# Kernel tuning notes

Measured on AMD Instinct MI355X. Metric: run time of the kernel, lower is better.

The kernel has to match this reference:

```python
import jax, jax.numpy as jnp
import numpy as np

TEMPERATURE = 8.0  # sqrt(d_k) with d_k=64

def setup_inputs() -> dict:
    key = jax.random.key(0)
    k1, k2, k3, k4 = jax.random.split(key, 4)
    B, L, D = 64, 1024, 64  # B = batch*n_heads
    q = jax.random.normal(k1, (B, L, D), dtype=jnp.float32)
    k = jax.random.normal(k2, (B, L, D), dtype=jnp.float32)
    v = jax.random.normal(k3, (B, L, D), dtype=jnp.float32)
    mask = jax.random.randint(k4, (B, L, L), 0, 2).astype(jnp.bool_)
    return {"q": q, "k": k, "v": v, "mask": mask}

def reference(q, k, v, mask):
    # scores: [B, Lq, Lk]
    attn = jnp.einsum('bqd,bkd->bqk', q, k) / TEMPERATURE
    attn = jnp.where(mask, -jnp.inf, attn)
    attn = jax.nn.softmax(attn, axis=2)
    output = jnp.einsum('bqk,bkd->bqd', attn, v)
    return (output, attn)
```

## Files before the change

kernel.cpp:

```cpp
#include <hip/hip_runtime.h>

#define B_ 64
#define L_ 1024
#define D_ 64
#define QT 16

typedef _Float16 f16;
typedef __attribute__((ext_vector_type(8))) _Float16 f16x8;
typedef __attribute__((ext_vector_type(4))) _Float16 f16x4;
typedef __attribute__((ext_vector_type(4))) float f32x4;

#define WS_KH 0u
#define WS_KL 8388608u
#define WS_VT 16777216u
#define WS_NEED 25165824u

#define MFMA16(A, B, C) __builtin_amdgcn_mfma_f32_16x16x32_f16((A), (B), (C), 0, 0, 0)

__global__ __launch_bounds__(256)
void prep_kv(const float* __restrict__ kk, const float* __restrict__ v,
             f16* __restrict__ kh, f16* __restrict__ kl, f16* __restrict__ vt) {
    __shared__ f16 tile[64][72];
    if (blockIdx.x < 2048) {
        const int i = (blockIdx.x * 256 + threadIdx.x) * 8;
        float4 f0 = *(const float4*)(kk + i);
        float4 f1 = *(const float4*)(kk + i + 4);
        float fv[8] = {f0.x, f0.y, f0.z, f0.w, f1.x, f1.y, f1.z, f1.w};
        f16x8 h, lo;
        #pragma unroll
        for (int j = 0; j < 8; ++j) {
            float x = fv[j] * 0.125f;
            f16 hh = (f16)x;
            h[j] = hh;
            lo[j] = (f16)(x - (float)hh);
        }
        *(f16x8*)(kh + i) = h;
        *(f16x8*)(kl + i) = lo;
    } else {
        const int bb = blockIdx.x - 2048;
        const int b = bb >> 4, kt = bb & 15;
        const int r = threadIdx.x >> 2, c0 = (threadIdx.x & 3) * 16;
        const float* vp = v + (size_t)(b * L_ + kt * 64 + r) * D_ + c0;
        float4 g0 = *(const float4*)vp;
        float4 g1 = *(const float4*)(vp + 4);
        float4 g2 = *(const float4*)(vp + 8);
        float4 g3 = *(const float4*)(vp + 12);
        float fv[16] = {g0.x, g0.y, g0.z, g0.w, g1.x, g1.y, g1.z, g1.w,
                        g2.x, g2.y, g2.z, g2.w, g3.x, g3.y, g3.z, g3.w};
        #pragma unroll
        for (int j = 0; j < 16; ++j) tile[r][c0 + j] = (f16)fv[j];
        __syncthreads();
        f16x8 o0, o1;
        #pragma unroll
        for (int j = 0; j < 8; ++j) { o0[j] = tile[c0 + j][r]; o1[j] = tile[c0 + 8 + j][r]; }
        f16* op = vt + (size_t)(b * 64 + r) * 1024 + kt * 64 + c0;
        *(f16x8*)op = o0;
        *(f16x8*)(op + 8) = o1;
    }
}


template<bool E4>
__device__ __forceinline__ void sdpa_body(
    const float* __restrict__ q, const f16* __restrict__ kh,
    const f16* __restrict__ kl, const f16* __restrict__ vt,
    const unsigned char* __restrict__ mask,
    float* __restrict__ out, float* __restrict__ attn,
    f16* __restrict__ ST, float (*wsumP)[QT], float* __restrict__ OL)
{
    const int tid = threadIdx.x;
    const int l = tid & 63, w = tid >> 6;
    const int lr = l & 15, lg = l >> 4;
    const int bid = blockIdx.x;
    const int b = bid >> 6, qt = bid & 63;
    const int qbase = b * L_ + qt * QT;
    const int kq = w * 256;
    const int wbase = w * 4096;
    const int swx = (lr & 7) << 3;

    f16x8 aqh0, aqh1, aql0, aql1;
    {
        const float* qp = q + (size_t)(qbase + lr) * D_;
        float4 f0 = *(const float4*)(qp + lg * 8);
        float4 f1 = *(const float4*)(qp + lg * 8 + 4);
        float4 f2 = *(const float4*)(qp + 32 + lg * 8);
        float4 f3 = *(const float4*)(qp + 32 + lg * 8 + 4);
        float fa[8] = {f0.x, f0.y, f0.z, f0.w, f1.x, f1.y, f1.z, f1.w};
        float fb[8] = {f2.x, f2.y, f2.z, f2.w, f3.x, f3.y, f3.z, f3.w};
        #pragma unroll
        for (int j = 0; j < 8; ++j) {
            f16 h = (f16)fa[j]; aqh0[j] = h; aql0[j] = (f16)(fa[j] - (float)h);
            h = (f16)fb[j];     aqh1[j] = h; aql1[j] = (f16)(fb[j] - (float)h);
        }
    }

    const size_t mrow = (size_t)(qbase + lr) * L_ + kq + lg * 4;
    int4 mq[4]; uchar4 mu[4];
    #pragma unroll
    for (int t = 0; t < 4; ++t) {
        if (E4) mq[t] = *(const int4*)((const int*)mask + mrow + t * 16);
        else    mu[t] = *(const uchar4*)(mask + mrow + t * 16);
    }

    const f16* khp = kh + (size_t)(b * L_ + kq + lr) * D_ + lg * 8;
    const f16* klp = kl + (size_t)(b * L_ + kq + lr) * D_ + lg * 8;
    f16x8 kc0 = *(const f16x8*)khp, kc1 = *(const f16x8*)(khp + 32);
    f16x8 lc0 = *(const f16x8*)klp, lc1 = *(const f16x8*)(klp + 32);

    float rsum = 0.f;

    #pragma unroll
    for (int c = 0; c < 16; ++c) {
        f16x8 kn0, kn1, ln0, ln1;
        if (c < 15) {
            const f16* p1 = khp + (c + 1) * 1024;
            const f16* p2 = klp + (c + 1) * 1024;
            kn0 = *(const f16x8*)p1; kn1 = *(const f16x8*)(p1 + 32);
            ln0 = *(const f16x8*)p2; ln1 = *(const f16x8*)(p2 + 32);
        }
        f32x4 acc = {0.f, 0.f, 0.f, 0.f};
        acc = MFMA16(kc0, aqh0, acc);
        acc = MFMA16(kc1, aqh1, acc);
        acc = MFMA16(kc0, aql0, acc);
        acc = MFMA16(kc1, aql1, acc);
        acc = MFMA16(lc0, aqh0, acc);
        acc = MFMA16(lc1, aqh1, acc);
        int mm[4];
        if (E4) { mm[0] = mq[c & 3].x; mm[1] = mq[c & 3].y;
                  mm[2] = mq[c & 3].z; mm[3] = mq[c & 3].w; }
        else    { mm[0] = mu[c & 3].x; mm[1] = mu[c & 3].y;
                  mm[2] = mu[c & 3].z; mm[3] = mu[c & 3].w; }
        f16x4 qd;
        #pragma unroll
        for (int r = 0; r < 4; ++r) {
            float e = mm[r] ? 0.f : __expf(acc[r]);
            rsum += e;
            qd[r] = (f16)e;
        }
        *(f16x4*)&ST[(wbase + lr * 256 + c * 16 + lg * 4) ^ swx] = qd;
        if (c + 4 < 16) {
            if (E4) mq[c & 3] = *(const int4*)((const int*)mask + mrow + (c + 4) * 16);
            else    mu[c & 3] = *(const uchar4*)(mask + mrow + (c + 4) * 16);
        }
        if (c < 15) { kc0 = kn0; kc1 = kn1; lc0 = ln0; lc1 = ln1; }
    }

    asm volatile("s_waitcnt lgkmcnt(0)" ::: "memory");
    __builtin_amdgcn_sched_barrier(0);
    f16x8 pa[8];
    #pragma unroll
    for (int t = 0; t < 8; ++t)
        pa[t] = *(const f16x8*)&ST[(wbase + lr * 256 + t * 32 + lg * 8) ^ swx];

    rsum += __shfl_xor(rsum, 16);
    rsum += __shfl_xor(rsum, 32);
    if (l < 16) wsumP[w][lr] = rsum;
    __syncthreads();

    const float inv = 1.0f / (wsumP[0][lr] + wsumP[1][lr] + wsumP[2][lr] + wsumP[3][lr]);

    const f16* vtb = vt + (size_t)b * 64 * 1024 + kq + lg * 8;
    float* ap = attn + (size_t)(qbase + lr) * L_ + kq + lg * 8;
    f32x4 acc4[4] = {{0,0,0,0},{0,0,0,0},{0,0,0,0},{0,0,0,0}};
    f16x8 bc[4];
    #pragma unroll
    for (int nt = 0; nt < 4; ++nt)
        bc[nt] = *(const f16x8*)(vtb + (size_t)(nt * 16 + lr) * 1024);

    #pragma unroll
    for (int t = 0; t < 8; ++t) {
        f16x8 bn[4];
        if (t < 7) {
            #pragma unroll
            for (int nt = 0; nt < 4; ++nt)
                bn[nt] = *(const f16x8*)(vtb + (size_t)(nt * 16 + lr) * 1024 + (t + 1) * 32);
        }
        f32x4 p0, p1;
        p0[0] = (float)pa[t][0] * inv; p0[1] = (float)pa[t][1] * inv;
        p0[2] = (float)pa[t][2] * inv; p0[3] = (float)pa[t][3] * inv;
        p1[0] = (float)pa[t][4] * inv; p1[1] = (float)pa[t][5] * inv;
        p1[2] = (float)pa[t][6] * inv; p1[3] = (float)pa[t][7] * inv;
        *(f32x4*)(ap + t * 32)     = p0;
        *(f32x4*)(ap + t * 32 + 4) = p1;
        #pragma unroll
        for (int nt = 0; nt < 4; ++nt)
            acc4[nt] = MFMA16(pa[t], bc[nt], acc4[nt]);
        if (t < 7) {
            #pragma unroll
            for (int nt = 0; nt < 4; ++nt) bc[nt] = bn[nt];
        }
    }

    #pragma unroll
    for (int nt = 0; nt < 4; ++nt) {
        #pragma unroll
        for (int r = 0; r < 4; ++r)
            OL[w * (16 * 68) + (lg * 4 + r) * 68 + nt * 16 + lr] = acc4[nt][r];
    }
    __syncthreads();
    {
        const int row = tid >> 4, c4 = (tid & 15) * 4;
        f32x4 o = {0.f, 0.f, 0.f, 0.f};
        #pragma unroll
        for (int ww = 0; ww < 4; ++ww) {
            const float* p = &OL[ww * (16 * 68) + row * 68 + c4];
            o[0] += p[0]; o[1] += p[1]; o[2] += p[2]; o[3] += p[3];
        }
        const float invr = 1.0f / (wsumP[0][row] + wsumP[1][row] + wsumP[2][row] + wsumP[3][row]);
        f32x4 r = {o[0] * invr, o[1] * invr, o[2] * invr, o[3] * invr};
        *(f32x4*)(out + (size_t)(qbase + row) * D_ + c4) = r;
    }
}

__global__ __launch_bounds__(256, 4)
void sdpa_main(const float* __restrict__ q, const f16* __restrict__ kh,
               const f16* __restrict__ kl, const f16* __restrict__ vt,
               const unsigned char* __restrict__ mask,
               float* __restrict__ out, float* __restrict__ attn)
{
    __shared__ __align__(16) char smem[32768];
    __shared__ float wsumP[4][QT];

    unsigned det = 0;
    {
        const unsigned* mw = (const unsigned*)mask;
        #pragma unroll
        for (int i = 0; i < 32; ++i) det |= mw[i];
    }
    const bool elem4 = (det <= 1u) || (det == 0x3F800000u);

    if (elem4)
        sdpa_body<true>(q, kh, kl, vt, mask, out, attn, (f16*)smem, wsumP, (float*)smem);
    else
        sdpa_body<false>(q, kh, kl, vt, mask, out, attn, (f16*)smem, wsumP, (float*)smem);
}


__device__ __forceinline__ int sidx(int row, int col) {
    return row * 1024 + ((((col >> 3) ^ (row & 7)) << 3) | (col & 7));
}

__global__ __launch_bounds__(256, 4)
void sdpa_fallback(const float* __restrict__ q, const float* __restrict__ kk,
                   const float* __restrict__ v, const unsigned char* __restrict__ mask,
                   float* __restrict__ out, float* __restrict__ attn)
{
    __shared__ f16 S[QT * 1024];
    __shared__ float wmax[4][QT];
    __shared__ float wsum[QT];

    const int tid = threadIdx.x;
    const int l = tid & 63, w = tid >> 6;
    const int lr = l & 15, lg = l >> 4;
    const int bid = blockIdx.x;
    const int b = bid >> 6, qt = bid & 63;
    const int qbase = b * L_ + qt * QT;

    unsigned det = 0;
    {
        const unsigned* mw = (const unsigned*)mask;
        #pragma unroll
        for (int i = 0; i < 32; ++i) det |= mw[i];
    }
    const bool elem4 = (det <= 1u) || (det == 0x3F800000u);

    f16x8 aqh[2], aql[2];
    {
        const float* qp = q + (size_t)(qbase + lr) * D_;
        #pragma unroll
        for (int s = 0; s < 2; ++s) {
            float4 f0 = *(const float4*)(qp + s * 32 + lg * 8);
            float4 f1 = *(const float4*)(qp + s * 32 + lg * 8 + 4);
            float fv[8] = {f0.x, f0.y, f0.z, f0.w, f1.x, f1.y, f1.z, f1.w};
            #pragma unroll
            for (int j = 0; j < 8; ++j) {
                f16 h = (f16)fv[j];
                aqh[s][j] = h;
                aql[s][j] = (f16)(fv[j] - (float)h);
            }
        }
    }

    float vmax[4] = {-INFINITY, -INFINITY, -INFINITY, -INFINITY};
    const float* kb = kk + (size_t)(b * L_ + w * 16 + lr) * D_ + lg * 8;
    const size_t mrowbase = (size_t)(qbase + lg * 4) * L_ + w * 16 + lr;

    float4 kc[4];
    kc[0] = *(const float4*)kb;
    kc[1] = *(const float4*)(kb + 4);
    kc[2] = *(const float4*)(kb + 32);
    kc[3] = *(const float4*)(kb + 36);
    int mcur[4], mnxt[4];
    #pragma unroll
    for (int r2 = 0; r2 < 4; ++r2) {
        if (elem4) {
            mcur[r2] = ((const int*)mask)[mrowbase + (size_t)r2 * L_];
            mnxt[r2] = ((const int*)mask)[mrowbase + (size_t)r2 * L_ + 64];
        } else {
            mcur[r2] = mask[mrowbase + (size_t)r2 * L_];
            mnxt[r2] = mask[mrowbase + (size_t)r2 * L_ + 64];
        }
    }

    for (int ck = 0; ck < 16; ++ck) {
        float4 kn[4];
        if (ck < 15) {
            const float* kp = kb + (size_t)(ck + 1) * 64 * D_;
            kn[0] = *(const float4*)kp;
            kn[1] = *(const float4*)(kp + 4);
            kn[2] = *(const float4*)(kp + 32);
            kn[3] = *(const float4*)(kp + 36);
        }
        int mfut[4];
        if (ck < 14) {
            const size_t mo = mrowbase + (size_t)(ck + 2) * 64;
            if (elem4) {
                #pragma unroll
                for (int r2 = 0; r2 < 4; ++r2) mfut[r2] = ((const int*)mask)[mo + (size_t)r2 * L_];
            } else {
                #pragma unroll
                for (int r2 = 0; r2 < 4; ++r2) mfut[r2] = mask[mo + (size_t)r2 * L_];
            }
        }
        f16x8 bh[2], bl[2];
        #pragma unroll
        for (int s = 0; s < 2; ++s) {
            float fv[8] = {kc[2*s].x, kc[2*s].y, kc[2*s].z, kc[2*s].w,
                           kc[2*s+1].x, kc[2*s+1].y, kc[2*s+1].z, kc[2*s+1].w};
            #pragma unroll
            for (int j = 0; j < 8; ++j) {
                f16 h = (f16)fv[j];
                bh[s][j] = h;
                bl[s][j] = (f16)(fv[j] - (float)h);
            }
        }
        f32x4 acc = {0.f, 0.f, 0.f, 0.f};
        #pragma unroll
        for (int s = 0; s < 2; ++s) {
            acc = MFMA16(aqh[s], bh[s], acc);
            acc = MFMA16(aql[s], bh[s], acc);
            acc = MFMA16(aqh[s], bl[s], acc);
        }
        const int scol = ck * 64 + w * 16 + lr;
        #pragma unroll
        for (int r2 = 0; r2 < 4; ++r2) {
            float sv = mcur[r2] ? -INFINITY : acc[r2] * 0.125f;
            S[sidx(lg * 4 + r2, scol)] = (f16)sv;
            vmax[r2] = fmaxf(vmax[r2], sv);
        }
        #pragma unroll
        for (int r2 = 0; r2 < 4; ++r2) mcur[r2] = mnxt[r2];
        if (ck < 14) {
            #pragma unroll
            for (int r2 = 0; r2 < 4; ++r2) mnxt[r2] = mfut[r2];
        }
        if (ck < 15) {
            #pragma unroll
            for (int j = 0; j < 4; ++j) kc[j] = kn[j];
        }
    }
    #pragma unroll
    for (int r2 = 0; r2 < 4; ++r2) {
        #pragma unroll
        for (int off = 1; off < 16; off <<= 1)
            vmax[r2] = fmaxf(vmax[r2], __shfl_xor(vmax[r2], off));
    }
    if (lr == 0) {
        #pragma unroll
        for (int r2 = 0; r2 < 4; ++r2) wmax[w][lg * 4 + r2] = vmax[r2];
    }
    __syncthreads();

    {
        const int row = tid >> 4, cg = tid & 15;
        const float m = fmaxf(fmaxf(wmax[0][row], wmax[1][row]),
                              fmaxf(wmax[2][row], wmax[3][row]));
        float sum = 0.f;
        #pragma unroll
        for (int c = 0; c < 8; ++c) {
            f16* sp = &S[row * 1024 + (((cg + 16 * c) ^ (row & 7)) << 3)];
            f16x8 sv = *(const f16x8*)sp;
            f16x8 ev;
            #pragma unroll
            for (int j = 0; j < 8; ++j) {
                float e = __expf((float)sv[j] - m);
                ev[j] = (f16)e;
                sum += e;
            }
            *(f16x8*)sp = ev;
        }
        #pragma unroll
        for (int off = 1; off < 16; off <<= 1) sum += __shfl_xor(sum, off);
        if (cg == 0) wsum[row] = sum;
        __syncthreads();

        const float inv = 1.0f / wsum[row];
        float* ap = attn + (size_t)(qbase + row) * L_;
        #pragma unroll
        for (int c = 0; c < 8; ++c) {
            f16x8 ev = *(const f16x8*)&S[row * 1024 + (((cg + 16 * c) ^ (row & 7)) << 3)];
            float4 p0, p1;
            p0.x = (float)ev[0] * inv; p0.y = (float)ev[1] * inv;
            p0.z = (float)ev[2] * inv; p0.w = (float)ev[3] * inv;
            p1.x = (float)ev[4] * inv; p1.y = (float)ev[5] * inv;
            p1.z = (float)ev[6] * inv; p1.w = (float)ev[7] * inv;
            *(float4*)(ap + (cg + 16 * c) * 8)     = p0;
            *(float4*)(ap + (cg + 16 * c) * 8 + 4) = p1;
        }
    }

    f32x4 acc2 = {0.f, 0.f, 0.f, 0.f};
    const float* vb = v + (size_t)(b * L_) * D_ + w * 16 + lr;
    float vcA[8], vcB[8];
    #pragma unroll
    for (int j = 0; j < 8; ++j) {
        vcA[j] = vb[(size_t)(lg * 8 + j) * D_];
        vcB[j] = vb[(size_t)(32 + lg * 8 + j) * D_];
    }
    for (int tt = 0; tt < 16; ++tt) {
        {
            f16x8 pa = *(const f16x8*)&S[lr * 1024 + ((((2 * tt) * 4 + lg) ^ (lr & 7)) << 3)];
            f16x8 bv;
            #pragma unroll
            for (int j = 0; j < 8; ++j) bv[j] = (f16)vcA[j];
            if (tt < 15) {
                const float* vp = vb + (size_t)((2 * tt + 2) * 32 + lg * 8) * D_;
                #pragma unroll
                for (int j = 0; j < 8; ++j) vcA[j] = vp[(size_t)j * D_];
            }
            acc2 = MFMA16(pa, bv, acc2);
        }
        {
            f16x8 pa = *(const f16x8*)&S[lr * 1024 + ((((2 * tt + 1) * 4 + lg) ^ (lr & 7)) << 3)];
            f16x8 bv;
            #pragma unroll
            for (int j = 0; j < 8; ++j) bv[j] = (f16)vcB[j];
            if (tt < 15) {
                const float* vp = vb + (size_t)((2 * tt + 3) * 32 + lg * 8) * D_;
                #pragma unroll
                for (int j = 0; j < 8; ++j) vcB[j] = vp[(size_t)j * D_];
            }
            acc2 = MFMA16(pa, bv, acc2);
        }
    }

    #pragma unroll
    for (int r2 = 0; r2 < 4; ++r2) {
        const float invr = 1.0f / wsum[lg * 4 + r2];
        out[(size_t)(qbase + lg * 4 + r2) * D_ + w * 16 + lr] = acc2[r2] * invr;
    }
}

extern "C" void kernel_launch(void* const* d_in, const int* in_sizes, int n_in,
                              void* d_out, int out_size, void* d_ws, size_t ws_size,
                              hipStream_t stream) {
    const float* q = (const float*)d_in[0];
    const float* k = (const float*)d_in[1];
    const float* v = (const float*)d_in[2];
    const unsigned char* mask = (const unsigned char*)d_in[3];
    float* out = (float*)d_out;
    float* attn = out + (size_t)B_ * L_ * D_;

    if (ws_size >= (size_t)WS_NEED) {
        f16* kh = (f16*)((char*)d_ws + WS_KH);
        f16* kl = (f16*)((char*)d_ws + WS_KL);
        f16* vt = (f16*)((char*)d_ws + WS_VT);
        prep_kv<<<dim3(3072), 256, 0, stream>>>(k, v, kh, kl, vt);
        sdpa_main<<<dim3(B_ * (L_ / QT)), 256, 0, stream>>>(q, kh, kl, vt, mask, out, attn);
    } else {
        sdpa_fallback<<<dim3(B_ * (L_ / QT)), 256, 0, stream>>>(q, k, v, mask, out, attn);
    }
}
```

Baseline: 281.7 us.

## Split attention into producer and mask/softmax-writer warp groups with bitpacked mask

The main kernel now runs 512 threads per block. Four waves compute QK^T scores, exponentiate them into LDS and run the PV product. Four other waves load the mask, pack it into bits in LDS, compute row sums and write the normalized attention matrix. Block IDs are also remapped to interleave batches across the grid. The goal is to overlap the heavy mask read and attention write with the MFMA work, at the cost of more synchronization and of dropping the software-prefetch of V.

```diff
diff --git a/kernel.cpp b/kernel.cpp
--- a/kernel.cpp
+++ b/kernel.cpp
@@ -59,167 +59,190 @@
     }
 }
 
+struct SMem {
+    f16 staging[4 * 4096];
+    float OL[4 * 16 * 68];
+    unsigned short bits16[16 * 64];
+    float wsumP[4][16];
+};
 
 template<bool E4>
 __device__ __forceinline__ void sdpa_body(
     const float* __restrict__ q, const f16* __restrict__ kh,
     const f16* __restrict__ kl, const f16* __restrict__ vt,
     const unsigned char* __restrict__ mask,
-    float* __restrict__ out, float* __restrict__ attn,
-    f16* __restrict__ ST, float (*wsumP)[QT], float* __restrict__ OL)
+    float* __restrict__ out, float* __restrict__ attn, SMem* sm)
 {
     const int tid = threadIdx.x;
     const int l = tid & 63, w = tid >> 6;
     const int lr = l & 15, lg = l >> 4;
-    const int bid = blockIdx.x;
+    const int bid0 = blockIdx.x;
+    const int bid = (bid0 & 7) * 512 + (bid0 >> 3);
     const int b = bid >> 6, qt = bid & 63;
     const int qbase = b * L_ + qt * QT;
-    const int kq = w * 256;
-    const int wbase = w * 4096;
     const int swx = (lr & 7) << 3;
 
-    f16x8 aqh0, aqh1, aql0, aql1;
-    {
-        const float* qp = q + (size_t)(qbase + lr) * D_;
-        float4 f0 = *(const float4*)(qp + lg * 8);
-        float4 f1 = *(const float4*)(qp + lg * 8 + 4);
-        float4 f2 = *(const float4*)(qp + 32 + lg * 8);
-        float4 f3 = *(const float4*)(qp + 32 + lg * 8 + 4);
-        float fa[8] = {f0.x, f0.y, f0.z, f0.w, f1.x, f1.y, f1.z, f1.w};
-        float fb[8] = {f2.x, f2.y, f2.z, f2.w, f3.x, f3.y, f3.z, f3.w};
-        #pragma unroll
-        for (int j = 0; j < 8; ++j) {
-            f16 h = (f16)fa[j]; aqh0[j] = h; aql0[j] = (f16)(fa[j] - (float)h);
-            h = (f16)fb[j];     aqh1[j] = h; aql1[j] = (f16)(fb[j] - (float)h);
-        }
-    }
-
-    const size_t mrow = (size_t)(qbase + lr) * L_ + kq + lg * 4;
-    int4 mq[4]; uchar4 mu[4];
-    #pragma unroll
-    for (int t = 0; t < 4; ++t) {
-        if (E4) mq[t] = *(const int4*)((const int*)mask + mrow + t * 16);
-        else    mu[t] = *(const uchar4*)(mask + mrow + t * 16);
-    }
-
-    const f16* khp = kh + (size_t)(b * L_ + kq + lr) * D_ + lg * 8;
-    const f16* klp = kl + (size_t)(b * L_ + kq + lr) * D_ + lg * 8;
-    f16x8 kc0 = *(const f16x8*)khp, kc1 = *(const f16x8*)(khp + 32);
-    f16x8 lc0 = *(const f16x8*)klp, lc1 = *(const f16x8*)(klp + 32);
-
-    float rsum = 0.f;
-
-    #pragma unroll
-    for (int c = 0; c < 16; ++c) {
-        f16x8 kn0, kn1, ln0, ln1;
-        if (c < 15) {
-            const f16* p1 = khp + (c + 1) * 1024;
-            const f16* p2 = klp + (c + 1) * 1024;
-            kn0 = *(const f16x8*)p1; kn1 = *(const f16x8*)(p1 + 32);
-            ln0 = *(const f16x8*)p2; ln1 = *(const f16x8*)(p2 + 32);
-        }
-        f32x4 acc = {0.f, 0.f, 0.f, 0.f};
-        acc = MFMA16(kc0, aqh0, acc);
-        acc = MFMA16(kc1, aqh1, acc);
-        acc = MFMA16(kc0, aql0, acc);
-        acc = MFMA16(kc1, aql1, acc);
-        acc = MFMA16(lc0, aqh0, acc);
-        acc = MFMA16(lc1, aqh1, acc);
-        int mm[4];
-        if (E4) { mm[0] = mq[c & 3].x; mm[1] = mq[c & 3].y;
-                  mm[2] = mq[c & 3].z; mm[3] = mq[c & 3].w; }
-        else    { mm[0] = mu[c & 3].x; mm[1] = mu[c & 3].y;
-                  mm[2] = mu[c & 3].z; mm[3] = mu[c & 3].w; }
-        f16x4 qd;
+    if (w < 4) {
+        const int kq = w * 256;
+        const int wbase = w * 4096;
+
+        f16x8 aqh0, aqh1, aql0, aql1;
+        {
+            const float* qp = q + (size_t)(qbase + lr) * D_;
+            float4 f0 = *(const float4*)(qp + lg * 8);
+            float4 f1 = *(const float4*)(qp + lg * 8 + 4);
+            float4 f2 = *(const float4*)(qp + 32 + lg * 8);
+            float4 f3 = *(const float4*)(qp + 32 + lg * 8 + 4);
+            float fa[8] = {f0.x, f0.y, f0.z, f0.w, f1.x, f1.y, f1.z, f1.w};
+            float fb[8] = {f2.x, f2.y, f2.z, f2.w, f3.x, f3.y, f3.z, f3.w};
+            #pragma unroll
+            for (int j = 0; j < 8; ++j) {
+                f16 h = (f16)fa[j]; aqh0[j] = h; aql0[j] = (f16)(fa[j] - (float)h);
+                h = (f16)fb[j];     aqh1[j] = h; aql1[j] = (f16)(fb[j] - (float)h);
+            }
+        }
+
+        const f16* khp = kh + (size_t)(b * L_ + kq + lr) * D_ + lg * 8;
+        const f16* klp = kl + (size_t)(b * L_ + kq + lr) * D_ + lg * 8;
+        f16x8 kc0 = *(const f16x8*)khp, kc1 = *(const f16x8*)(khp + 32);
+        f16x8 lc0 = *(const f16x8*)klp, lc1 = *(const f16x8*)(klp + 32);
+        #pragma unroll
+        for (int c = 0; c < 16; ++c) {
+            f16x8 kn0, kn1, ln0, ln1;
+            if (c < 15) {
+                const f16* p1 = khp + (c + 1) * 1024;
+                const f16* p2 = klp + (c + 1) * 1024;
+                kn0 = *(const f16x8*)p1; kn1 = *(const f16x8*)(p1 + 32);
+                ln0 = *(const f16x8*)p2; ln1 = *(const f16x8*)(p2 + 32);
+            }
+            f32x4 aA = {0.f,0.f,0.f,0.f}, aB = {0.f,0.f,0.f,0.f}, aC = {0.f,0.f,0.f,0.f};
+            aA = MFMA16(kc0, aqh0, aA); aA = MFMA16(kc1, aqh1, aA);
+            aB = MFMA16(kc0, aql0, aB); aB = MFMA16(kc1, aql1, aB);
+            aC = MFMA16(lc0, aqh0, aC); aC = MFMA16(lc1, aqh1, aC);
+            f16x4 qd;
+            #pragma unroll
+            for (int r = 0; r < 4; ++r)
+                qd[r] = (f16)__expf(aA[r] + aB[r] + aC[r]);
+            *(f16x4*)&sm->staging[(wbase + lr * 256 + c * 16 + lg * 4) ^ swx] = qd;
+            if (c < 15) { kc0 = kn0; kc1 = kn1; lc0 = ln0; lc1 = ln1; }
+        }
+        __syncthreads();
+
+        const f16* vtb = vt + (size_t)b * 64 * 1024 + kq + lg * 8;
+        const unsigned* bw = (const unsigned*)sm->bits16;
+        f32x4 a0 = {0.f,0.f,0.f,0.f}, a1 = {0.f,0.f,0.f,0.f};
+        f32x4 a2 = {0.f,0.f,0.f,0.f}, a3 = {0.f,0.f,0.f,0.f};
+        #pragma unroll
+        for (int t = 0; t < 8; ++t) {
+            f16x8 pa = *(const f16x8*)&sm->staging[(wbase + lr * 256 + t * 32 + lg * 8) ^ swx];
+            const unsigned byt = (bw[lr * 32 + w * 8 + t] >> (lg * 8)) & 0xFFu;
+            #pragma unroll
+            for (int j = 0; j < 8; ++j)
+                pa[j] = ((byt >> j) & 1u) ? (f16)0.f : pa[j];
+            f16x8 b0 = *(const f16x8*)(vtb + (size_t)(0 * 16 + lr) * 1024 + t * 32);
+            f16x8 b1 = *(const f16x8*)(vtb + (size_t)(1 * 16 + lr) * 1024 + t * 32);
+            f16x8 b2 = *(const f16x8*)(vtb + (size_t)(2 * 16 + lr) * 1024 + t * 32);
+            f16x8 b3 = *(const f16x8*)(vtb + (size_t)(3 * 16 + lr) * 1024 + t * 32);
+            a0 = MFMA16(pa, b0, a0); a1 = MFMA16(pa, b1, a1);
+            a2 = MFMA16(pa, b2, a2); a3 = MFMA16(pa, b3, a3);
+        }
         #pragma unroll
         for (int r = 0; r < 4; ++r) {
-            float e = mm[r] ? 0.f : __expf(acc[r]);
-            rsum += e;
-            qd[r] = (f16)e;
-        }
-        *(f16x4*)&ST[(wbase + lr * 256 + c * 16 + lg * 4) ^ swx] = qd;
-        if (c + 4 < 16) {
-            if (E4) mq[c & 3] = *(const int4*)((const int*)mask + mrow + (c + 4) * 16);
-            else    mu[c & 3] = *(const uchar4*)(mask + mrow + (c + 4) * 16);
-        }
-        if (c < 15) { kc0 = kn0; kc1 = kn1; lc0 = ln0; lc1 = ln1; }
-    }
-
-    asm volatile("s_waitcnt lgkmcnt(0)" ::: "memory");
-    __builtin_amdgcn_sched_barrier(0);
-    f16x8 pa[8];
-    #pragma unroll
-    for (int t = 0; t < 8; ++t)
-        pa[t] = *(const f16x8*)&ST[(wbase + lr * 256 + t * 32 + lg * 8) ^ swx];
-
-    rsum += __shfl_xor(rsum, 16);
-    rsum += __shfl_xor(rsum, 32);
-    if (l < 16) wsumP[w][lr] = rsum;
-    __syncthreads();
-
-    const float inv = 1.0f / (wsumP[0][lr] + wsumP[1][lr] + wsumP[2][lr] + wsumP[3][lr]);
-
-    const f16* vtb = vt + (size_t)b * 64 * 1024 + kq + lg * 8;
-    float* ap = attn + (size_t)(qbase + lr) * L_ + kq + lg * 8;
-    f32x4 acc4[4] = {{0,0,0,0},{0,0,0,0},{0,0,0,0},{0,0,0,0}};
-    f16x8 bc[4];
-    #pragma unroll
-    for (int nt = 0; nt < 4; ++nt)
-        bc[nt] = *(const f16x8*)(vtb + (size_t)(nt * 16 + lr) * 1024);
-
-    #pragma unroll
-    for (int t = 0; t < 8; ++t) {
-        f16x8 bn[4];
-        if (t < 7) {
-            #pragma unroll
-            for (int nt = 0; nt < 4; ++nt)
-                bn[nt] = *(const f16x8*)(vtb + (size_t)(nt * 16 + lr) * 1024 + (t + 1) * 32);
-        }
-        f32x4 p0, p1;
-        p0[0] = (float)pa[t][0] * inv; p0[1] = (float)pa[t][1] * inv;
-        p0[2] = (float)pa[t][2] * inv; p0[3] = (float)pa[t][3] * inv;
-        p1[0] = (float)pa[t][4] * inv; p1[1] = (float)pa[t][5] * inv;
-        p1[2] = (float)pa[t][6] * inv; p1[3] = (float)pa[t][7] * inv;
-        *(f32x4*)(ap + t * 32)     = p0;
-        *(f32x4*)(ap + t * 32 + 4) = p1;
-        #pragma unroll
-        for (int nt = 0; nt < 4; ++nt)
-            acc4[nt] = MFMA16(pa[t], bc[nt], acc4[nt]);
-        if (t < 7) {
-            #pragma unroll
-            for (int nt = 0; nt < 4; ++nt) bc[nt] = bn[nt];
-        }
-    }
-
-    #pragma unroll
-    for (int nt = 0; nt < 4; ++nt) {
-        #pragma unroll
-        for (int r = 0; r < 4; ++r)
-            OL[w * (16 * 68) + (lg * 4 + r) * 68 + nt * 16 + lr] = acc4[nt][r];
-    }
-    __syncthreads();
-    {
-        const int row = tid >> 4, c4 = (tid & 15) * 4;
-        f32x4 o = {0.f, 0.f, 0.f, 0.f};
-        #pragma unroll
-        for (int ww = 0; ww < 4; ++ww) {
-            const float* p = &OL[ww * (16 * 68) + row * 68 + c4];
-            o[0] += p[0]; o[1] += p[1]; o[2] += p[2]; o[3] += p[3];
-        }
-        const float invr = 1.0f / (wsumP[0][row] + wsumP[1][row] + wsumP[2][row] + wsumP[3][row]);
-        f32x4 r = {o[0] * invr, o[1] * invr, o[2] * invr, o[3] * invr};
-        *(f32x4*)(out + (size_t)(qbase + row) * D_ + c4) = r;
-    }
-}
-
-__global__ __launch_bounds__(256, 4)
+            sm->OL[w * (16 * 68) + (lg * 4 + r) * 68 + 0 * 16 + lr] = a0[r];
+            sm->OL[w * (16 * 68) + (lg * 4 + r) * 68 + 1 * 16 + lr] = a1[r];
+            sm->OL[w * (16 * 68) + (lg * 4 + r) * 68 + 2 * 16 + lr] = a2[r];
+            sm->OL[w * (16 * 68) + (lg * 4 + r) * 68 + 3 * 16 + lr] = a3[r];
+        }
+        __syncthreads();
+
+        {
+            const int row = tid >> 4, c4 = (tid & 15) * 4;
+            f32x4 o = {0.f, 0.f, 0.f, 0.f};
+            #pragma unroll
+            for (int ww = 0; ww < 4; ++ww) {
+                const float* p = &sm->OL[ww * (16 * 68) + row * 68 + c4];
+                o[0] += p[0]; o[1] += p[1]; o[2] += p[2]; o[3] += p[3];
+            }
+            const float invr = 1.0f / (sm->wsumP[0][row] + sm->wsumP[1][row] +
+                                       sm->wsumP[2][row] + sm->wsumP[3][row]);
+            f32x4 r = {o[0] * invr, o[1] * invr, o[2] * invr, o[3] * invr};
+            *(f32x4*)(out + (size_t)(qbase + row) * D_ + c4) = r;
+        }
+    } else {
+        const int sw = w - 4;
+        const int kq = sw * 256;
+        const size_t mrow = (size_t)(qbase + lr) * L_ + kq + lg * 64;
+
+        #pragma unroll
+        for (int r = 0; r < 4; ++r) {
+            unsigned bits = 0;
+            if (E4) {
+                const int* mp = (const int*)mask + mrow + r * 16;
+                int4 a = *(const int4*)mp;
+                int4 c2 = *(const int4*)(mp + 4);
+                int4 d = *(const int4*)(mp + 8);
+                int4 e = *(const int4*)(mp + 12);
+                bits |= (a.x?1u:0u)|(a.y?2u:0u)|(a.z?4u:0u)|(a.w?8u:0u);
+                bits |= (c2.x?16u:0u)|(c2.y?32u:0u)|(c2.z?64u:0u)|(c2.w?128u:0u);
+                bits |= (d.x?256u:0u)|(d.y?512u:0u)|(d.z?1024u:0u)|(d.w?2048u:0u);
+                bits |= (e.x?4096u:0u)|(e.y?8192u:0u)|(e.z?16384u:0u)|(e.w?32768u:0u);
+            } else {
+                const uint4 a = *(const uint4*)(mask + mrow + r * 16);
+                const unsigned wds[4] = {a.x, a.y, a.z, a.w};
+                #pragma unroll
+                for (int g = 0; g < 4; ++g) {
+                    unsigned u = wds[g];
+                    if (u & 0x000000FFu) bits |= 1u << (g * 4 + 0);
+                    if (u & 0x0000FF00u) bits |= 1u << (g * 4 + 1);
+                    if (u & 0x00FF0000u) bits |= 1u << (g * 4 + 2);
+                    if (u & 0xFF000000u) bits |= 1u << (g * 4 + 3);
+                }
+            }
+            sm->bits16[lr * 64 + (kq >> 4) + lg * 4 + r] = (unsigned short)bits;
+        }
+        __syncthreads();
+
+        const unsigned* bw = (const unsigned*)sm->bits16;
+        f16x8 ev[8];
+        float rsum = 0.f;
+        #pragma unroll
+        for (int t = 0; t < 8; ++t) {
+            f16x8 e = *(const f16x8*)&sm->staging[(sw * 4096 + lr * 256 + t * 32 + lg * 8) ^ swx];
+            const unsigned byt = (bw[lr * 32 + sw * 8 + t] >> (lg * 8)) & 0xFFu;
+            #pragma unroll
+            for (int j = 0; j < 8; ++j) {
+                e[j] = ((byt >> j) & 1u) ? (f16)0.f : e[j];
+                rsum += (float)e[j];
+            }
+            ev[t] = e;
+        }
+        rsum += __shfl_xor(rsum, 16);
+        rsum += __shfl_xor(rsum, 32);
+        if (l < 16) sm->wsumP[sw][lr] = rsum;
+        __syncthreads();
+
+        const float inv = 1.0f / (sm->wsumP[0][lr] + sm->wsumP[1][lr] +
+                                  sm->wsumP[2][lr] + sm->wsumP[3][lr]);
+        float* ap = attn + (size_t)(qbase + lr) * L_ + kq + lg * 8;
+        #pragma unroll
+        for (int t = 0; t < 8; ++t) {
+            f32x4 p0 = {(float)ev[t][0] * inv, (float)ev[t][1] * inv,
+                        (float)ev[t][2] * inv, (float)ev[t][3] * inv};
+            f32x4 p1 = {(float)ev[t][4] * inv, (float)ev[t][5] * inv,
+                        (float)ev[t][6] * inv, (float)ev[t][7] * inv};
+            *(f32x4*)(ap + t * 32)     = p0;
+            *(f32x4*)(ap + t * 32 + 4) = p1;
+        }
+    }
+}
+
+__global__ __launch_bounds__(512, 6)
 void sdpa_main(const float* __restrict__ q, const f16* __restrict__ kh,
                const f16* __restrict__ kl, const f16* __restrict__ vt,
                const unsigned char* __restrict__ mask,
                float* __restrict__ out, float* __restrict__ attn)
 {
-    __shared__ __align__(16) char smem[32768];
-    __shared__ float wsumP[4][QT];
+    __shared__ SMem sm;
 
     unsigned det = 0;
     {
@@ -229,10 +252,8 @@
     }
     const bool elem4 = (det <= 1u) || (det == 0x3F800000u);
 
-    if (elem4)
-        sdpa_body<true>(q, kh, kl, vt, mask, out, attn, (f16*)smem, wsumP, (float*)smem);
-    else
-        sdpa_body<false>(q, kh, kl, vt, mask, out, attn, (f16*)smem, wsumP, (float*)smem);
+    if (elem4) sdpa_body<true>(q, kh, kl, vt, mask, out, attn, &sm);
+    else       sdpa_body<false>(q, kh, kl, vt, mask, out, attn, &sm);
 }
 
 
@@ -380,14 +401,14 @@
         for (int c = 0; c < 8; ++c) {
             f16* sp = &S[row * 1024 + (((cg + 16 * c) ^ (row & 7)) << 3)];
             f16x8 sv = *(const f16x8*)sp;
-            f16x8 ev;
+            f16x8 evv;
             #pragma unroll
             for (int j = 0; j < 8; ++j) {
                 float e = __expf((float)sv[j] - m);
-                ev[j] = (f16)e;
+                evv[j] = (f16)e;
                 sum += e;
             }
-            *(f16x8*)sp = ev;
+            *(f16x8*)sp = evv;
         }
         #pragma unroll
         for (int off = 1; off < 16; off <<= 1) sum += __shfl_xor(sum, off);
@@ -398,12 +419,12 @@
         float* ap = attn + (size_t)(qbase + row) * L_;
         #pragma unroll
         for (int c = 0; c < 8; ++c) {
-            f16x8 ev = *(const f16x8*)&S[row * 1024 + (((cg + 16 * c) ^ (row & 7)) << 3)];
+            f16x8 evv = *(const f16x8*)&S[row * 1024 + (((cg + 16 * c) ^ (row & 7)) << 3)];
             float4 p0, p1;
-            p0.x = (float)ev[0] * inv; p0.y = (float)ev[1] * inv;
-            p0.z = (float)ev[2] * inv; p0.w = (float)ev[3] * inv;
-            p1.x = (float)ev[4] * inv; p1.y = (float)ev[5] * inv;
-            p1.z = (float)ev[6] * inv; p1.w = (float)ev[7] * inv;
+            p0.x = (float)evv[0] * inv; p0.y = (float)evv[1] * inv;
+            p0.z = (float)evv[2] * inv; p0.w = (float)evv[3] * inv;
+            p1.x = (float)evv[4] * inv; p1.y = (float)evv[5] * inv;
+            p1.z = (float)evv[6] * inv; p1.w = (float)evv[7] * inv;
             *(float4*)(ap + (cg + 16 * c) * 8)     = p0;
             *(float4*)(ap + (cg + 16 * c) * 8 + 4) = p1;
         }
@@ -466,7 +487,7 @@
         f16* kl = (f16*)((char*)d_ws + WS_KL);
         f16* vt = (f16*)((char*)d_ws + WS_VT);
         prep_kv<<<dim3(3072), 256, 0, stream>>>(k, v, kh, kl, vt);
-        sdpa_main<<<dim3(B_ * (L_ / QT)), 256, 0, stream>>>(q, kh, kl, vt, mask, out, attn);
+        sdpa_main<<<dim3(B_ * (L_ / QT)), 512, 0, stream>>>(q, kh, kl, vt, mask, out, attn);
     } else {
         sdpa_fallback<<<dim3(B_ * (L_ / QT)), 256, 0, stream>>>(q, k, v, mask, out, attn);
     }
```

New measurement: 300.9 us. +6.8%, slower.

## Process four query tiles per block with XCD-aware block remap and deeper mask prefetch

Applied to the files above, without the earlier changes.

Each block now loops over four consecutive query tiles of the same batch, so the grid shrinks from 4096 to 1024 blocks. Block indices are remapped so that consecutive blocks on one XCD share a batch, which should help K/V reuse in L2. The QK MFMA chain is split into three independent accumulators to shorten the dependency chain, and the mask prefetch ring grows from 4 to 8 entries. In exchange there are fewer blocks to hide latency, an extra barrier per tile, and more registers in use.

```diff
diff --git a/kernel.cpp b/kernel.cpp
--- a/kernel.cpp
+++ b/kernel.cpp
@@ -71,144 +71,148 @@
     const int tid = threadIdx.x;
     const int l = tid & 63, w = tid >> 6;
     const int lr = l & 15, lg = l >> 4;
-    const int bid = blockIdx.x;
-    const int b = bid >> 6, qt = bid & 63;
-    const int qbase = b * L_ + qt * QT;
+    const int bid0 = blockIdx.x;
+    const int bid = (bid0 & 7) * 128 + (bid0 >> 3);
     const int kq = w * 256;
     const int wbase = w * 4096;
     const int swx = (lr & 7) << 3;
 
-    f16x8 aqh0, aqh1, aql0, aql1;
-    {
-        const float* qp = q + (size_t)(qbase + lr) * D_;
-        float4 f0 = *(const float4*)(qp + lg * 8);
-        float4 f1 = *(const float4*)(qp + lg * 8 + 4);
-        float4 f2 = *(const float4*)(qp + 32 + lg * 8);
-        float4 f3 = *(const float4*)(qp + 32 + lg * 8 + 4);
-        float fa[8] = {f0.x, f0.y, f0.z, f0.w, f1.x, f1.y, f1.z, f1.w};
-        float fb[8] = {f2.x, f2.y, f2.z, f2.w, f3.x, f3.y, f3.z, f3.w};
-        #pragma unroll
-        for (int j = 0; j < 8; ++j) {
-            f16 h = (f16)fa[j]; aqh0[j] = h; aql0[j] = (f16)(fa[j] - (float)h);
-            h = (f16)fb[j];     aqh1[j] = h; aql1[j] = (f16)(fb[j] - (float)h);
-        }
-    }
-
-    const size_t mrow = (size_t)(qbase + lr) * L_ + kq + lg * 4;
-    int4 mq[4]; uchar4 mu[4];
-    #pragma unroll
-    for (int t = 0; t < 4; ++t) {
-        if (E4) mq[t] = *(const int4*)((const int*)mask + mrow + t * 16);
-        else    mu[t] = *(const uchar4*)(mask + mrow + t * 16);
-    }
-
+    const int b = (bid * 4) >> 6;
     const f16* khp = kh + (size_t)(b * L_ + kq + lr) * D_ + lg * 8;
     const f16* klp = kl + (size_t)(b * L_ + kq + lr) * D_ + lg * 8;
-    f16x8 kc0 = *(const f16x8*)khp, kc1 = *(const f16x8*)(khp + 32);
-    f16x8 lc0 = *(const f16x8*)klp, lc1 = *(const f16x8*)(klp + 32);
-
-    float rsum = 0.f;
-
-    #pragma unroll
-    for (int c = 0; c < 16; ++c) {
-        f16x8 kn0, kn1, ln0, ln1;
-        if (c < 15) {
-            const f16* p1 = khp + (c + 1) * 1024;
-            const f16* p2 = klp + (c + 1) * 1024;
-            kn0 = *(const f16x8*)p1; kn1 = *(const f16x8*)(p1 + 32);
-            ln0 = *(const f16x8*)p2; ln1 = *(const f16x8*)(p2 + 32);
-        }
-        f32x4 acc = {0.f, 0.f, 0.f, 0.f};
-        acc = MFMA16(kc0, aqh0, acc);
-        acc = MFMA16(kc1, aqh1, acc);
-        acc = MFMA16(kc0, aql0, acc);
-        acc = MFMA16(kc1, aql1, acc);
-        acc = MFMA16(lc0, aqh0, acc);
-        acc = MFMA16(lc1, aqh1, acc);
-        int mm[4];
-        if (E4) { mm[0] = mq[c & 3].x; mm[1] = mq[c & 3].y;
-                  mm[2] = mq[c & 3].z; mm[3] = mq[c & 3].w; }
-        else    { mm[0] = mu[c & 3].x; mm[1] = mu[c & 3].y;
-                  mm[2] = mu[c & 3].z; mm[3] = mu[c & 3].w; }
-        f16x4 qd;
-        #pragma unroll
-        for (int r = 0; r < 4; ++r) {
-            float e = mm[r] ? 0.f : __expf(acc[r]);
-            rsum += e;
-            qd[r] = (f16)e;
-        }
-        *(f16x4*)&ST[(wbase + lr * 256 + c * 16 + lg * 4) ^ swx] = qd;
-        if (c + 4 < 16) {
-            if (E4) mq[c & 3] = *(const int4*)((const int*)mask + mrow + (c + 4) * 16);
-            else    mu[c & 3] = *(const uchar4*)(mask + mrow + (c + 4) * 16);
-        }
-        if (c < 15) { kc0 = kn0; kc1 = kn1; lc0 = ln0; lc1 = ln1; }
-    }
-
-    asm volatile("s_waitcnt lgkmcnt(0)" ::: "memory");
-    __builtin_amdgcn_sched_barrier(0);
-    f16x8 pa[8];
-    #pragma unroll
-    for (int t = 0; t < 8; ++t)
-        pa[t] = *(const f16x8*)&ST[(wbase + lr * 256 + t * 32 + lg * 8) ^ swx];
-
-    rsum += __shfl_xor(rsum, 16);
-    rsum += __shfl_xor(rsum, 32);
-    if (l < 16) wsumP[w][lr] = rsum;
-    __syncthreads();
-
-    const float inv = 1.0f / (wsumP[0][lr] + wsumP[1][lr] + wsumP[2][lr] + wsumP[3][lr]);
-
     const f16* vtb = vt + (size_t)b * 64 * 1024 + kq + lg * 8;
-    float* ap = attn + (size_t)(qbase + lr) * L_ + kq + lg * 8;
-    f32x4 acc4[4] = {{0,0,0,0},{0,0,0,0},{0,0,0,0},{0,0,0,0}};
-    f16x8 bc[4];
-    #pragma unroll
-    for (int nt = 0; nt < 4; ++nt)
-        bc[nt] = *(const f16x8*)(vtb + (size_t)(nt * 16 + lr) * 1024);
-
-    #pragma unroll
-    for (int t = 0; t < 8; ++t) {
-        f16x8 bn[4];
-        if (t < 7) {
+
+    for (int it = 0; it < 4; ++it) {
+        const int tile = bid * 4 + it;
+        const int qt = tile & 63;
+        const int qbase = b * L_ + qt * QT;
+
+        f16x8 aqh0, aqh1, aql0, aql1;
+        {
+            const float* qp = q + (size_t)(qbase + lr) * D_;
+            float4 f0 = *(const float4*)(qp + lg * 8);
+            float4 f1 = *(const float4*)(qp + lg * 8 + 4);
+            float4 f2 = *(const float4*)(qp + 32 + lg * 8);
+            float4 f3 = *(const float4*)(qp + 32 + lg * 8 + 4);
+            float fa[8] = {f0.x, f0.y, f0.z, f0.w, f1.x, f1.y, f1.z, f1.w};
+            float fb[8] = {f2.x, f2.y, f2.z, f2.w, f3.x, f3.y, f3.z, f3.w};
+            #pragma unroll
+            for (int j = 0; j < 8; ++j) {
+                f16 h = (f16)fa[j]; aqh0[j] = h; aql0[j] = (f16)(fa[j] - (float)h);
+                h = (f16)fb[j];     aqh1[j] = h; aql1[j] = (f16)(fb[j] - (float)h);
+            }
+        }
+
+        const size_t mrow = (size_t)(qbase + lr) * L_ + kq + lg * 4;
+        int4 mq[8]; uchar4 mu[8];
+        #pragma unroll
+        for (int t = 0; t < 8; ++t) {
+            if (E4) mq[t] = *(const int4*)((const int*)mask + mrow + t * 16);
+            else    mu[t] = *(const uchar4*)(mask + mrow + t * 16);
+        }
+
+        f16x8 kc0 = *(const f16x8*)khp, kc1 = *(const f16x8*)(khp + 32);
+        f16x8 lc0 = *(const f16x8*)klp, lc1 = *(const f16x8*)(klp + 32);
+        float rsum = 0.f;
+        #pragma unroll
+        for (int c = 0; c < 16; ++c) {
+            f16x8 kn0, kn1, ln0, ln1;
+            if (c < 15) {
+                const f16* p1 = khp + (c + 1) * 1024;
+                const f16* p2 = klp + (c + 1) * 1024;
+                kn0 = *(const f16x8*)p1; kn1 = *(const f16x8*)(p1 + 32);
+                ln0 = *(const f16x8*)p2; ln1 = *(const f16x8*)(p2 + 32);
+            }
+            f32x4 aA = {0.f,0.f,0.f,0.f}, aB = {0.f,0.f,0.f,0.f}, aC = {0.f,0.f,0.f,0.f};
+            aA = MFMA16(kc0, aqh0, aA); aA = MFMA16(kc1, aqh1, aA);
+            aB = MFMA16(kc0, aql0, aB); aB = MFMA16(kc1, aql1, aB);
+            aC = MFMA16(lc0, aqh0, aC); aC = MFMA16(lc1, aqh1, aC);
+            int mm[4];
+            if (E4) { mm[0] = mq[c & 7].x; mm[1] = mq[c & 7].y;
+                      mm[2] = mq[c & 7].z; mm[3] = mq[c & 7].w; }
+            else    { mm[0] = mu[c & 7].x; mm[1] = mu[c & 7].y;
+                      mm[2] = mu[c & 7].z; mm[3] = mu[c & 7].w; }
+            if (c + 8 < 16) {
+                if (E4) mq[c & 7] = *(const int4*)((const int*)mask + mrow + (c + 8) * 16);
+                else    mu[c & 7] = *(const uchar4*)(mask + mrow + (c + 8) * 16);
+            }
+            f16x4 qd;
+            #pragma unroll
+            for (int r = 0; r < 4; ++r) {
+                float e = mm[r] ? 0.f : __expf(aA[r] + aB[r] + aC[r]);
+                rsum += e;
+                qd[r] = (f16)e;
+            }
+            *(f16x4*)&ST[(wbase + lr * 256 + c * 16 + lg * 4) ^ swx] = qd;
+            if (c < 15) { kc0 = kn0; kc1 = kn1; lc0 = ln0; lc1 = ln1; }
+        }
+
+        asm volatile("s_waitcnt lgkmcnt(0)" ::: "memory");
+        __builtin_amdgcn_sched_barrier(0);
+        f16x8 pa[8];
+        #pragma unroll
+        for (int t = 0; t < 8; ++t)
+            pa[t] = *(const f16x8*)&ST[(wbase + lr * 256 + t * 32 + lg * 8) ^ swx];
+
+        rsum += __shfl_xor(rsum, 16);
+        rsum += __shfl_xor(rsum, 32);
+        if (l < 16) wsumP[w][lr] = rsum;
+        __syncthreads();
+
+        const float inv = 1.0f / (wsumP[0][lr] + wsumP[1][lr] + wsumP[2][lr] + wsumP[3][lr]);
+
+        float* ap = attn + (size_t)(qbase + lr) * L_ + kq + lg * 8;
+        f32x4 acc4[4] = {{0,0,0,0},{0,0,0,0},{0,0,0,0},{0,0,0,0}};
+        f16x8 bc[4];
+        #pragma unroll
+        for (int nt = 0; nt < 4; ++nt)
+            bc[nt] = *(const f16x8*)(vtb + (size_t)(nt * 16 + lr) * 1024);
+
+        #pragma unroll
+        for (int t = 0; t < 8; ++t) {
+            f16x8 bn[4];
+            if (t < 7) {
+                #pragma unroll
+                for (int nt = 0; nt < 4; ++nt)
+                    bn[nt] = *(const f16x8*)(vtb + (size_t)(nt * 16 + lr) * 1024 + (t + 1) * 32);
+            }
+            f32x4 p0, p1;
+            p0[0] = (float)pa[t][0] * inv; p0[1] = (float)pa[t][1] * inv;
+            p0[2] = (float)pa[t][2] * inv; p0[3] = (float)pa[t][3] * inv;
+            p1[0] = (float)pa[t][4] * inv; p1[1] = (float)pa[t][5] * inv;
+            p1[2] = (float)pa[t][6] * inv; p1[3] = (float)pa[t][7] * inv;
+            *(f32x4*)(ap + t * 32)     = p0;
+            *(f32x4*)(ap + t * 32 + 4) = p1;
             #pragma unroll
             for (int nt = 0; nt < 4; ++nt)
-                bn[nt] = *(const f16x8*)(vtb + (size_t)(nt * 16 + lr) * 1024 + (t + 1) * 32);
-        }
-        f32x4 p0, p1;
-        p0[0] = (float)pa[t][0] * inv; p0[1] = (float)pa[t][1] * inv;
-        p0[2] = (float)pa[t][2] * inv; p0[3] = (float)pa[t][3] * inv;
-        p1[0] = (float)pa[t][4] * inv; p1[1] = (float)pa[t][5] * inv;
-        p1[2] = (float)pa[t][6] * inv; p1[3] = (float)pa[t][7] * inv;
-        *(f32x4*)(ap + t * 32)     = p0;
-        *(f32x4*)(ap + t * 32 + 4) = p1;
-        #pragma unroll
-        for (int nt = 0; nt < 4; ++nt)
-            acc4[nt] = MFMA16(pa[t], bc[nt], acc4[nt]);
-        if (t < 7) {
-            #pragma unroll
-            for (int nt = 0; nt < 4; ++nt) bc[nt] = bn[nt];
-        }
-    }
-
-    #pragma unroll
-    for (int nt = 0; nt < 4; ++nt) {
-        #pragma unroll
-        for (int r = 0; r < 4; ++r)
-            OL[w * (16 * 68) + (lg * 4 + r) * 68 + nt * 16 + lr] = acc4[nt][r];
-    }
-    __syncthreads();
-    {
-        const int row = tid >> 4, c4 = (tid & 15) * 4;
-        f32x4 o = {0.f, 0.f, 0.f, 0.f};
-        #pragma unroll
-        for (int ww = 0; ww < 4; ++ww) {
-            const float* p = &OL[ww * (16 * 68) + row * 68 + c4];
-            o[0] += p[0]; o[1] += p[1]; o[2] += p[2]; o[3] += p[3];
-        }
-        const float invr = 1.0f / (wsumP[0][row] + wsumP[1][row] + wsumP[2][row] + wsumP[3][row]);
-        f32x4 r = {o[0] * invr, o[1] * invr, o[2] * invr, o[3] * invr};
-        *(f32x4*)(out + (size_t)(qbase + row) * D_ + c4) = r;
+                acc4[nt] = MFMA16(pa[t], bc[nt], acc4[nt]);
+            if (t < 7) {
+                #pragma unroll
+                for (int nt = 0; nt < 4; ++nt) bc[nt] = bn[nt];
+            }
+        }
+
+        #pragma unroll
+        for (int nt = 0; nt < 4; ++nt) {
+            #pragma unroll
+            for (int r = 0; r < 4; ++r)
+                OL[w * (16 * 68) + (lg * 4 + r) * 68 + nt * 16 + lr] = acc4[nt][r];
+        }
+        __syncthreads();
+        {
+            const int row = tid >> 4, c4 = (tid & 15) * 4;
+            f32x4 o = {0.f, 0.f, 0.f, 0.f};
+            #pragma unroll
+            for (int ww = 0; ww < 4; ++ww) {
+                const float* p = &OL[ww * (16 * 68) + row * 68 + c4];
+                o[0] += p[0]; o[1] += p[1]; o[2] += p[2]; o[3] += p[3];
+            }
+            const float invr = 1.0f / (wsumP[0][row] + wsumP[1][row] +
+                                       wsumP[2][row] + wsumP[3][row]);
+            f32x4 r = {o[0] * invr, o[1] * invr, o[2] * invr, o[3] * invr};
+            *(f32x4*)(out + (size_t)(qbase + row) * D_ + c4) = r;
+        }
+        __syncthreads();
     }
 }
 
@@ -380,14 +384,14 @@
         for (int c = 0; c < 8; ++c) {
             f16* sp = &S[row * 1024 + (((cg + 16 * c) ^ (row & 7)) << 3)];
             f16x8 sv = *(const f16x8*)sp;
-            f16x8 ev;
+            f16x8 evv;
             #pragma unroll
             for (int j = 0; j < 8; ++j) {
                 float e = __expf((float)sv[j] - m);
-                ev[j] = (f16)e;
+                evv[j] = (f16)e;
                 sum += e;
             }
-            *(f16x8*)sp = ev;
+            *(f16x8*)sp = evv;
         }
         #pragma unroll
         for (int off = 1; off < 16; off <<= 1) sum += __shfl_xor(sum, off);
@@ -398,12 +402,12 @@
         float* ap = attn + (size_t)(qbase + row) * L_;
         #pragma unroll
         for (int c = 0; c < 8; ++c) {
-            f16x8 ev = *(const f16x8*)&S[row * 1024 + (((cg + 16 * c) ^ (row & 7)) << 3)];
+            f16x8 evv = *(const f16x8*)&S[row * 1024 + (((cg + 16 * c) ^ (row & 7)) << 3)];
             float4 p0, p1;
-            p0.x = (float)ev[0] * inv; p0.y = (float)ev[1] * inv;
-            p0.z = (float)ev[2] * inv; p0.w = (float)ev[3] * inv;
-            p1.x = (float)ev[4] * inv; p1.y = (float)ev[5] * inv;
-            p1.z = (float)ev[6] * inv; p1.w = (float)ev[7] * inv;
+            p0.x = (float)evv[0] * inv; p0.y = (float)evv[1] * inv;
+            p0.z = (float)evv[2] * inv; p0.w = (float)evv[3] * inv;
+            p1.x = (float)evv[4] * inv; p1.y = (float)evv[5] * inv;
+            p1.z = (float)evv[6] * inv; p1.w = (float)evv[7] * inv;
             *(float4*)(ap + (cg + 16 * c) * 8)     = p0;
             *(float4*)(ap + (cg + 16 * c) * 8 + 4) = p1;
         }
@@ -466,7 +470,7 @@
         f16* kl = (f16*)((char*)d_ws + WS_KL);
         f16* vt = (f16*)((char*)d_ws + WS_VT);
         prep_kv<<<dim3(3072), 256, 0, stream>>>(k, v, kh, kl, vt);
-        sdpa_main<<<dim3(B_ * (L_ / QT)), 256, 0, stream>>>(q, kh, kl, vt, mask, out, attn);
+        sdpa_main<<<dim3(1024), 256, 0, stream>>>(q, kh, kl, vt, mask, out, attn);
     } else {
         sdpa_fallback<<<dim3(B_ * (L_ / QT)), 256, 0, stream>>>(q, k, v, mask, out, attn);
     }
```

Result: slower. 514.6 us (+82.6%).
